# Kernel tuning notes

Measured on AMD Instinct MI355X. Metric: run time of the kernel, lower is better.

Reference implementation:

```python
import jax, jax.numpy as jnp
import numpy as np

N_NODES = 50000
N_EDGES = 800000
D_IN = 128
HID = 128
N_CLASSES = 2
N_GRAPHS = 500
N_LAYERS = 7


def setup_inputs() -> dict:
    key = jax.random.key(0)
    ks = jax.random.split(key, 8)
    x = jax.random.normal(ks[0], (N_NODES, D_IN), dtype=jnp.float32)
    edge_index = jax.random.randint(ks[1], (2, N_EDGES), 0, N_NODES, dtype=jnp.int32)
    batch = jnp.sort(jax.random.randint(ks[2], (N_NODES,), 0, N_GRAPHS, dtype=jnp.int32))
    s = 1.0 / np.sqrt(HID).astype(np.float32)
    # SAGEConv params: Wl (neighbor lin, with bias bl), Wr (root lin, no bias)
    Wl = jax.random.normal(ks[3], (N_LAYERS, HID, HID), dtype=jnp.float32) * s
    Wr = jax.random.normal(ks[4], (N_LAYERS, HID, HID), dtype=jnp.float32) * s
    bl = jnp.zeros((N_LAYERS, HID), dtype=jnp.float32)
    W_out = jax.random.normal(ks[5], (HID, N_CLASSES), dtype=jnp.float32) * s
    b_out = jnp.zeros((N_CLASSES,), dtype=jnp.float32)
    return {"x": x, "edge_index": edge_index, "batch": batch,
            "Wl": Wl, "Wr": Wr, "bl": bl, "W_out": W_out, "b_out": b_out}


def reference(x, edge_index, batch, Wl, Wr, bl, W_out, b_out):
    n = x.shape[0]
    src, dst = edge_index[0], edge_index[1]  # messages flow src -> dst
    deg = jax.ops.segment_sum(jnp.ones_like(dst, dtype=x.dtype), dst, num_segments=n)
    inv_deg = (1.0 / jnp.clip(deg, 1.0))[:, None]  # [N,1]; zero-degree -> aggregate stays 0

    def sage_layer(h, i):
        # mean aggregation of neighbor features, then linear + root linear
        agg = jax.ops.segment_sum(h[src], dst, num_segments=n) * inv_deg  # [N,H]
        return agg @ Wl[i] + bl[i] + h @ Wr[i]

    h = x
    for i in range(N_LAYERS - 1):
        h = jax.nn.relu(sage_layer(h, i))
    h = sage_layer(h, N_LAYERS - 1)  # last conv: no relu

    pooled = jax.ops.segment_sum(h, batch, num_segments=N_GRAPHS)  # global_add_pool
    # F.dropout with training=False is identity (eval mode)
    return pooled @ W_out + b_out  # [G, num_classes]
```

## Files before the change

### kernel.cpp

```cpp
#include <hip/hip_runtime.h>
#include <stdint.h>

#define NN 50000
#define NE 800000
#define HID 128
#define NG 500
#define NL 7

typedef short bf16x8 __attribute__((ext_vector_type(8)));
typedef float f32x4 __attribute__((ext_vector_type(4)));

__device__ __forceinline__ unsigned short f2bf(float f) {
  unsigned int u = __builtin_bit_cast(unsigned int, f);
  u += 0x7FFFu + ((u >> 16) & 1u);
  return (unsigned short)(u >> 16);
}
__device__ __forceinline__ float bf2f(unsigned short h) {
  unsigned int u = ((unsigned int)h) << 16;
  return __builtin_bit_cast(float, u);
}
__device__ __forceinline__ float bflo(unsigned int u) {
  return __builtin_bit_cast(float, u << 16);
}
__device__ __forceinline__ float bfhi(unsigned int u) {
  return __builtin_bit_cast(float, u & 0xffff0000u);
}

__global__ void k_pre(const float* __restrict__ x, unsigned short* __restrict__ hA,
                      unsigned short* __restrict__ hB,
                      const int* __restrict__ dstE, int* __restrict__ deg,
                      const float* __restrict__ Wl, const float* __restrict__ Wr,
                      unsigned short* __restrict__ wswh,
                      unsigned short* __restrict__ wswl) {
  int i = blockIdx.x * 256 + threadIdx.x;
  if (i < NN * HID / 4) {
    float4 v = ((const float4*)x)[i];
    ushort4 r;
    r.x = f2bf(v.x); r.y = f2bf(v.y); r.z = f2bf(v.z); r.w = f2bf(v.w);
    ((ushort4*)hA)[i] = r;
  }
  if (i < NE) atomicAdd(&deg[dstE[i]], 1);
  if (i < NL * 2 * 4 * 4096) {
    int j = i & 7, ii = (i >> 3) & 15, q = (i >> 7) & 3, t = (i >> 9) & 7;
    int cc = (i >> 12) & 3, m = (i >> 14) & 1, l = i >> 15;
    int k = cc * 32 + q * 8 + j, n = t * 16 + ii;
    const float* W = m ? Wr : Wl;
    float w = W[l * HID * HID + k * HID + n];
    unsigned short hi = f2bf(w);
    unsigned short lo = f2bf(w - bf2f(hi));
    wswh[i] = hi;
    wswl[i] = lo;
  }
  if (i < 2048) {
    int b = i >> 10, r = (i >> 4) & 63, u = i & 15;
    unsigned short* pad = (b ? hB : hA) + (size_t)(NN + r) * HID;
    *(uint4*)&pad[u * 8] = make_uint4(0u, 0u, 0u, 0u);
  }
}

__global__ void k_scan1(const int* __restrict__ deg, int* __restrict__ offs,
                        int* __restrict__ bsum) {
  int i = blockIdx.x * 256 + threadIdx.x;
  int v = (i < NN) ? deg[i] : 0;
  int lane = threadIdx.x & 63, wv = threadIdx.x >> 6;
  int x = v;
  #pragma unroll
  for (int d = 1; d < 64; d <<= 1) {
    int y = __shfl_up(x, d, 64);
    if (lane >= d) x += y;
  }
  __shared__ int wsum[4];
  if (lane == 63) wsum[wv] = x;
  __syncthreads();
  if (threadIdx.x == 0) {
    int s = 0;
    for (int k = 0; k < 4; k++) { int t = wsum[k]; wsum[k] = s; s += t; }
    bsum[blockIdx.x] = s;
  }
  __syncthreads();
  if (i < NN) offs[i] = x - v + wsum[wv];
}

__global__ void k_scan2(int* __restrict__ bsum, int nb) {
  int i = threadIdx.x;
  int v = (i < nb) ? bsum[i] : 0;
  int lane = threadIdx.x & 63, wv = threadIdx.x >> 6;
  int x = v;
  #pragma unroll
  for (int d = 1; d < 64; d <<= 1) {
    int y = __shfl_up(x, d, 64);
    if (lane >= d) x += y;
  }
  __shared__ int wsum[4];
  if (lane == 63) wsum[wv] = x;
  __syncthreads();
  if (threadIdx.x == 0) {
    int s = 0;
    for (int k = 0; k < 4; k++) { int t = wsum[k]; wsum[k] = s; s += t; }
  }
  __syncthreads();
  if (i < nb) bsum[i] = x - v + wsum[wv];
}

__global__ void k_scan3(const int* __restrict__ deg, int* __restrict__ offs,
                        const int* __restrict__ bsum, float* __restrict__ invd) {
  int i = blockIdx.x * 256 + threadIdx.x;
  if (i < NN) {
    offs[i] += bsum[blockIdx.x];
    int d = deg[i];
    invd[i] = 1.0f / (float)(d > 0 ? d : 1);
    if (i == 0) offs[NN] = NE;
  }
}

__global__ void k_fill(const int* __restrict__ src, const int* __restrict__ dst,
                       const int* __restrict__ offs, int* __restrict__ cur,
                       int* __restrict__ csr) {
  int e = blockIdx.x * 256 + threadIdx.x;
  if (e < NE) {
    int d = dst[e];
    int p = atomicAdd(&cur[d], 1);
    csr[offs[d] + p] = src[e];
  }
}

#define ACC8(V) { a0 += bflo(V.x); a1 += bfhi(V.x); a2 += bflo(V.y); \
                  a3 += bfhi(V.y); a4 += bflo(V.z); a5 += bfhi(V.z); \
                  a6 += bflo(V.w); a7 += bfhi(V.w); }

__global__ __launch_bounds__(256, 6) void k_agg(const unsigned short* __restrict__ curh,
                                                const int* __restrict__ offs,
                                                const int* __restrict__ csr,
                                                const float* __restrict__ invd,
                                                unsigned short* __restrict__ agg) {
  const int tid = threadIdx.x;
  const int qw = tid >> 4, sl = tid & 15;
  const int node = blockIdx.x * 16 + qw;
  const unsigned short* rowbase = curh + sl * 8;
  float a0 = 0.f, a1 = 0.f, a2 = 0.f, a3 = 0.f;
  float a4 = 0.f, a5 = 0.f, a6 = 0.f, a7 = 0.f;
  const int s = offs[node], e = offs[node + 1];
  for (int base = s; base < e; base += 16) {
    int idx = (base + sl < e) ? csr[base + sl] : NN;
    uint4 v0 = *(const uint4*)(rowbase + (size_t)__shfl(idx, 0, 16) * HID);
    uint4 v1 = *(const uint4*)(rowbase + (size_t)__shfl(idx, 1, 16) * HID);
    uint4 v2 = *(const uint4*)(rowbase + (size_t)__shfl(idx, 2, 16) * HID);
    uint4 v3 = *(const uint4*)(rowbase + (size_t)__shfl(idx, 3, 16) * HID);
    uint4 v4 = *(const uint4*)(rowbase + (size_t)__shfl(idx, 4, 16) * HID);
    uint4 v5 = *(const uint4*)(rowbase + (size_t)__shfl(idx, 5, 16) * HID);
    uint4 v6 = *(const uint4*)(rowbase + (size_t)__shfl(idx, 6, 16) * HID);
    uint4 v7 = *(const uint4*)(rowbase + (size_t)__shfl(idx, 7, 16) * HID);
    ACC8(v0) ACC8(v1) ACC8(v2) ACC8(v3) ACC8(v4) ACC8(v5) ACC8(v6) ACC8(v7)
    if (base + 8 < e) {
      v0 = *(const uint4*)(rowbase + (size_t)__shfl(idx,  8, 16) * HID);
      v1 = *(const uint4*)(rowbase + (size_t)__shfl(idx,  9, 16) * HID);
      v2 = *(const uint4*)(rowbase + (size_t)__shfl(idx, 10, 16) * HID);
      v3 = *(const uint4*)(rowbase + (size_t)__shfl(idx, 11, 16) * HID);
      v4 = *(const uint4*)(rowbase + (size_t)__shfl(idx, 12, 16) * HID);
      v5 = *(const uint4*)(rowbase + (size_t)__shfl(idx, 13, 16) * HID);
      v6 = *(const uint4*)(rowbase + (size_t)__shfl(idx, 14, 16) * HID);
      v7 = *(const uint4*)(rowbase + (size_t)__shfl(idx, 15, 16) * HID);
      ACC8(v0) ACC8(v1) ACC8(v2) ACC8(v3) ACC8(v4) ACC8(v5) ACC8(v6) ACC8(v7)
    }
  }
  float sc = invd[node];
  a0 *= sc; a1 *= sc; a2 *= sc; a3 *= sc;
  a4 *= sc; a5 *= sc; a6 *= sc; a7 *= sc;
  unsigned int w0 = (unsigned int)f2bf(a0) | ((unsigned int)f2bf(a1) << 16);
  unsigned int w1 = (unsigned int)f2bf(a2) | ((unsigned int)f2bf(a3) << 16);
  unsigned int w2 = (unsigned int)f2bf(a4) | ((unsigned int)f2bf(a5) << 16);
  unsigned int w3 = (unsigned int)f2bf(a6) | ((unsigned int)f2bf(a7) << 16);
  *(uint4*)(agg + (size_t)node * HID + sl * 8) = make_uint4(w0, w1, w2, w3);
}

__global__ __launch_bounds__(256) void k_gemm(const unsigned short* __restrict__ agg,
                                              const unsigned short* __restrict__ curh,
                                              const unsigned short* __restrict__ wswh,
                                              const unsigned short* __restrict__ wswl,
                                              const float* __restrict__ bias,
                                              unsigned short* __restrict__ out,
                                              int relu) {
  __shared__ __align__(16) unsigned short sW2[8192];
  const int tid = threadIdx.x;
  const int lane = tid & 63, wv = tid >> 6;
  const int row0 = blockIdx.x * 64;
  const int mr = (wv << 4) + (lane & 15);
  const int q = lane >> 4;
  const unsigned short* aRow = agg + (size_t)(row0 + mr) * HID + q * 8;
  const unsigned short* hRow = curh + (size_t)(row0 + mr) * HID + q * 8;

  f32x4 acc[8];
  #pragma unroll
  for (int t = 0; t < 8; t++) acc[t] = (f32x4){0.f, 0.f, 0.f, 0.f};

  for (int c = 0; c < 8; ++c) {
    const uint4* wh = (const uint4*)(wswh + c * 4096);
    const uint4* wl = (const uint4*)(wswl + c * 4096);
    ((uint4*)sW2)[tid] = wh[tid];
    ((uint4*)sW2)[tid + 256] = wh[tid + 256];
    ((uint4*)sW2)[tid + 512] = wl[tid];
    ((uint4*)sW2)[tid + 768] = wl[tid + 256];
    __syncthreads();
    bf16x8 a = *(const bf16x8*)(((c < 4) ? aRow : hRow) + (c & 3) * 32);
    #pragma unroll
    for (int t = 0; t < 8; t++) {
      bf16x8 bh = *(const bf16x8*)&sW2[(t * 4 + q) * 128 + (lane & 15) * 8];
      bf16x8 bl2 = *(const bf16x8*)&sW2[4096 + (t * 4 + q) * 128 + (lane & 15) * 8];
      acc[t] = __builtin_amdgcn_mfma_f32_16x16x32_bf16(a, bh, acc[t], 0, 0, 0);
      acc[t] = __builtin_amdgcn_mfma_f32_16x16x32_bf16(a, bl2, acc[t], 0, 0, 0);
    }
    __syncthreads();
  }

  const int ci = lane & 15;
  const int rb = (wv << 4) + (lane >> 4) * 4;
  #pragma unroll
  for (int t = 0; t < 8; t++) {
    int n = t * 16 + ci;
    float bn = bias[n];
    #pragma unroll
    for (int r2 = 0; r2 < 4; r2++) {
      int row = row0 + rb + r2;
      if (row < NN) {
        float v = acc[t][r2] + bn;
        if (relu) v = fmaxf(v, 0.f);
        out[(size_t)row * HID + n] = f2bf(v);
      }
    }
  }
}

__global__ void k_pool(const unsigned short* __restrict__ h,
                       const int* __restrict__ batch, float* __restrict__ pooled) {
  int g = blockIdx.x;
  __shared__ int rng[2];
  __shared__ float tmp[HID];
  if (threadIdx.x < 2) {
    int target = g + threadIdx.x;
    int lo = 0, hi = NN;
    while (lo < hi) {
      int mid = (lo + hi) >> 1;
      if (batch[mid] < target) lo = mid + 1; else hi = mid;
    }
    rng[threadIdx.x] = lo;
  }
  __syncthreads();
  int s = rng[0], e = rng[1];
  int f = threadIdx.x & 127, ro = threadIdx.x >> 7;
  float a = 0.f;
  for (int r = s + ro; r < e; r += 2) a += bf2f(h[(size_t)r * HID + f]);
  if (ro == 1) tmp[f] = a;
  __syncthreads();
  if (ro == 0) pooled[g * HID + f] = a + tmp[f];
}

__global__ void k_out(const float* __restrict__ pooled,
                      const float* __restrict__ Wout,
                      const float* __restrict__ bout,
                      float* __restrict__ out) {
  int g = blockIdx.x;
  int l = threadIdx.x;
  float a = pooled[g * HID + l], b = pooled[g * HID + 64 + l];
  float p0 = a * Wout[l * 2] + b * Wout[(l + 64) * 2];
  float p1 = a * Wout[l * 2 + 1] + b * Wout[(l + 64) * 2 + 1];
  #pragma unroll
  for (int d = 32; d; d >>= 1) {
    p0 += __shfl_down(p0, d, 64);
    p1 += __shfl_down(p1, d, 64);
  }
  if (l == 0) {
    out[g * 2] = p0 + bout[0];
    out[g * 2 + 1] = p1 + bout[1];
  }
}

extern "C" void kernel_launch(void* const* d_in, const int* in_sizes, int n_in,
                              void* d_out, int out_size, void* d_ws, size_t ws_size,
                              hipStream_t stream) {
  const float* x = (const float*)d_in[0];
  const int* ei = (const int*)d_in[1];
  const int* batch = (const int*)d_in[2];
  const float* Wl = (const float*)d_in[3];
  const float* Wr = (const float*)d_in[4];
  const float* bl = (const float*)d_in[5];
  const float* Wout = (const float*)d_in[6];
  const float* bout = (const float*)d_in[7];
  float* out = (float*)d_out;
  const int* srcE = ei;
  const int* dstE = ei + NE;

  char* w = (char*)d_ws;
  unsigned short* hA = (unsigned short*)w;  w += (size_t)(NN + 64) * HID * 2;
  unsigned short* hB = (unsigned short*)w;  w += (size_t)(NN + 64) * HID * 2;
  unsigned short* agg = (unsigned short*)w; w += (size_t)(NN + 64) * HID * 2;
  float* invd = (float*)w;   w += (size_t)NN * 4;
  float* pooled = (float*)w; w += (size_t)NG * HID * 4;
  int* deg = (int*)w;  w += (size_t)NN * 4;
  int* cur = (int*)w;  w += (size_t)NN * 4;
  int* offs = (int*)w; w += (size_t)50004 * 4;
  int* csr = (int*)w;  w += (size_t)NE * 4;
  int* bsum = (int*)w; w += 256 * 4;
  unsigned short* wswh = (unsigned short*)w; w += (size_t)NL * 2 * 4 * 4096 * 2;
  unsigned short* wswl = (unsigned short*)w;

  hipMemsetAsync(deg, 0, (size_t)NN * 2 * 4, stream);
  k_pre<<<(NN * HID / 4 + 255) / 256, 256, 0, stream>>>(x, hA, hB, dstE, deg,
                                                        Wl, Wr, wswh, wswl);
  int nb = (NN + 255) / 256;
  k_scan1<<<nb, 256, 0, stream>>>(deg, offs, bsum);
  k_scan2<<<1, 256, 0, stream>>>(bsum, nb);
  k_scan3<<<nb, 256, 0, stream>>>(deg, offs, bsum, invd);
  k_fill<<<(NE + 255) / 256, 256, 0, stream>>>(srcE, dstE, offs, cur, csr);

  unsigned short* curh = hA;
  unsigned short* nxth = hB;
  for (int l = 0; l < NL; l++) {
    k_agg<<<NN / 16, 256, 0, stream>>>(curh, offs, csr, invd, agg);
    k_gemm<<<(NN + 63) / 64, 256, 0, stream>>>(agg, curh,
                                               wswh + (size_t)l * 2 * 4 * 4096,
                                               wswl + (size_t)l * 2 * 4 * 4096,
                                               bl + l * HID, nxth,
                                               (l < NL - 1) ? 1 : 0);
    unsigned short* t = curh; curh = nxth; nxth = t;
  }
  k_pool<<<NG, 256, 0, stream>>>(curh, batch, pooled);
  k_out<<<NG, 64, 0, stream>>>(pooled, Wout, bout, out);
}
```

Before: 545.2 us.

## Partition CSR fill by destination range and issue all 16 gathers per chunk

The CSR fill kernel now splits its 1024 blocks into 128 edge chunks times 8 destination ranges. Each block scans its chunk and only scatters edges whose destination lies in its range, which keeps atomics and csr writes in a narrower address window, at the cost of reading dst eight times. The aggregation kernel now issues all 16 neighbor row loads unconditionally, relying on the padded sentinel row NN, to raise memory-level parallelism. Its occupancy hint drops from 6 to 4 to make room for the extra registers.

```diff
diff --git a/kernel.cpp b/kernel.cpp
--- a/kernel.cpp
+++ b/kernel.cpp
@@ -113,14 +113,20 @@
   }
 }
 
+#define FILL_CHUNK (NE / 128)
 __global__ void k_fill(const int* __restrict__ src, const int* __restrict__ dst,
                        const int* __restrict__ offs, int* __restrict__ cur,
                        int* __restrict__ csr) {
-  int e = blockIdx.x * 256 + threadIdx.x;
-  if (e < NE) {
+  const int r = blockIdx.x & 7;
+  const int chunk = blockIdx.x >> 3;
+  const int lo = r * (NN / 8), hi = lo + (NN / 8);
+  const int e0 = chunk * FILL_CHUNK;
+  for (int e = e0 + threadIdx.x; e < e0 + FILL_CHUNK; e += 256) {
     int d = dst[e];
-    int p = atomicAdd(&cur[d], 1);
-    csr[offs[d] + p] = src[e];
+    if (d >= lo && d < hi) {
+      int p = atomicAdd(&cur[d], 1);
+      csr[offs[d] + p] = src[e];
+    }
   }
 }
 
@@ -128,7 +134,7 @@
                   a3 += bfhi(V.y); a4 += bflo(V.z); a5 += bfhi(V.z); \
                   a6 += bflo(V.w); a7 += bfhi(V.w); }
 
-__global__ __launch_bounds__(256, 6) void k_agg(const unsigned short* __restrict__ curh,
+__global__ __launch_bounds__(256, 4) void k_agg(const unsigned short* __restrict__ curh,
                                                 const int* __restrict__ offs,
                                                 const int* __restrict__ csr,
                                                 const float* __restrict__ invd,
@@ -142,26 +148,26 @@
   const int s = offs[node], e = offs[node + 1];
   for (int base = s; base < e; base += 16) {
     int idx = (base + sl < e) ? csr[base + sl] : NN;
-    uint4 v0 = *(const uint4*)(rowbase + (size_t)__shfl(idx, 0, 16) * HID);
-    uint4 v1 = *(const uint4*)(rowbase + (size_t)__shfl(idx, 1, 16) * HID);
-    uint4 v2 = *(const uint4*)(rowbase + (size_t)__shfl(idx, 2, 16) * HID);
-    uint4 v3 = *(const uint4*)(rowbase + (size_t)__shfl(idx, 3, 16) * HID);
-    uint4 v4 = *(const uint4*)(rowbase + (size_t)__shfl(idx, 4, 16) * HID);
-    uint4 v5 = *(const uint4*)(rowbase + (size_t)__shfl(idx, 5, 16) * HID);
-    uint4 v6 = *(const uint4*)(rowbase + (size_t)__shfl(idx, 6, 16) * HID);
-    uint4 v7 = *(const uint4*)(rowbase + (size_t)__shfl(idx, 7, 16) * HID);
-    ACC8(v0) ACC8(v1) ACC8(v2) ACC8(v3) ACC8(v4) ACC8(v5) ACC8(v6) ACC8(v7)
-    if (base + 8 < e) {
-      v0 = *(const uint4*)(rowbase + (size_t)__shfl(idx,  8, 16) * HID);
-      v1 = *(const uint4*)(rowbase + (size_t)__shfl(idx,  9, 16) * HID);
-      v2 = *(const uint4*)(rowbase + (size_t)__shfl(idx, 10, 16) * HID);
-      v3 = *(const uint4*)(rowbase + (size_t)__shfl(idx, 11, 16) * HID);
-      v4 = *(const uint4*)(rowbase + (size_t)__shfl(idx, 12, 16) * HID);
-      v5 = *(const uint4*)(rowbase + (size_t)__shfl(idx, 13, 16) * HID);
-      v6 = *(const uint4*)(rowbase + (size_t)__shfl(idx, 14, 16) * HID);
-      v7 = *(const uint4*)(rowbase + (size_t)__shfl(idx, 15, 16) * HID);
-      ACC8(v0) ACC8(v1) ACC8(v2) ACC8(v3) ACC8(v4) ACC8(v5) ACC8(v6) ACC8(v7)
-    }
+    uint4 v0  = *(const uint4*)(rowbase + (size_t)__shfl(idx,  0, 16) * HID);
+    uint4 v1  = *(const uint4*)(rowbase + (size_t)__shfl(idx,  1, 16) * HID);
+    uint4 v2  = *(const uint4*)(rowbase + (size_t)__shfl(idx,  2, 16) * HID);
+    uint4 v3  = *(const uint4*)(rowbase + (size_t)__shfl(idx,  3, 16) * HID);
+    uint4 v4  = *(const uint4*)(rowbase + (size_t)__shfl(idx,  4, 16) * HID);
+    uint4 v5  = *(const uint4*)(rowbase + (size_t)__shfl(idx,  5, 16) * HID);
+    uint4 v6  = *(const uint4*)(rowbase + (size_t)__shfl(idx,  6, 16) * HID);
+    uint4 v7  = *(const uint4*)(rowbase + (size_t)__shfl(idx,  7, 16) * HID);
+    uint4 v8  = *(const uint4*)(rowbase + (size_t)__shfl(idx,  8, 16) * HID);
+    uint4 v9  = *(const uint4*)(rowbase + (size_t)__shfl(idx,  9, 16) * HID);
+    uint4 v10 = *(const uint4*)(rowbase + (size_t)__shfl(idx, 10, 16) * HID);
+    uint4 v11 = *(const uint4*)(rowbase + (size_t)__shfl(idx, 11, 16) * HID);
+    uint4 v12 = *(const uint4*)(rowbase + (size_t)__shfl(idx, 12, 16) * HID);
+    uint4 v13 = *(const uint4*)(rowbase + (size_t)__shfl(idx, 13, 16) * HID);
+    uint4 v14 = *(const uint4*)(rowbase + (size_t)__shfl(idx, 14, 16) * HID);
+    uint4 v15 = *(const uint4*)(rowbase + (size_t)__shfl(idx, 15, 16) * HID);
+    ACC8(v0)  ACC8(v1)  ACC8(v2)  ACC8(v3)
+    ACC8(v4)  ACC8(v5)  ACC8(v6)  ACC8(v7)
+    ACC8(v8)  ACC8(v9)  ACC8(v10) ACC8(v11)
+    ACC8(v12) ACC8(v13) ACC8(v14) ACC8(v15)
   }
   float sc = invd[node];
   a0 *= sc; a1 *= sc; a2 *= sc; a3 *= sc;
@@ -310,7 +316,7 @@
   k_scan1<<<nb, 256, 0, stream>>>(deg, offs, bsum);
   k_scan2<<<1, 256, 0, stream>>>(bsum, nb);
   k_scan3<<<nb, 256, 0, stream>>>(deg, offs, bsum, invd);
-  k_fill<<<(NE + 255) / 256, 256, 0, stream>>>(srcE, dstE, offs, cur, csr);
+  k_fill<<<1024, 256, 0, stream>>>(srcE, dstE, offs, cur, csr);
 
   unsigned short* curh = hA;
   unsigned short* nxth = hB;
```

Result: slower. 586.8 us (+7.6%).

## Fuse neighbor aggregation into GEMM kernel via LDS; partition CSR fill by dst range

Applied to the files above, without the earlier changes.

Merges the per-layer aggregation and GEMM kernels into one. Each 64-row block gathers its neighbor means into a swizzled LDS tile and feeds it straight to the MFMA loop, so the bf16 agg buffer is never written to or read back from global memory. The CSR fill now launches 1024 blocks that each scan a chunk of edges and handle only destinations in one eighth of the node range, which localizes the atomics and scattered writes. In exchange, the fused kernel uses 32KB of LDS per block and has fewer blocks than the old aggregation kernel. The fill step also reads the edge list eight times.

```diff
diff --git a/kernel.cpp b/kernel.cpp
--- a/kernel.cpp
+++ b/kernel.cpp
@@ -113,14 +113,20 @@
   }
 }
 
+#define FILL_CHUNK (NE / 128)
 __global__ void k_fill(const int* __restrict__ src, const int* __restrict__ dst,
                        const int* __restrict__ offs, int* __restrict__ cur,
                        int* __restrict__ csr) {
-  int e = blockIdx.x * 256 + threadIdx.x;
-  if (e < NE) {
+  const int r = blockIdx.x & 7;
+  const int chunk = blockIdx.x >> 3;
+  const int lo = r * (NN / 8), hi = lo + (NN / 8);
+  const int e0 = chunk * FILL_CHUNK;
+  for (int e = e0 + threadIdx.x; e < e0 + FILL_CHUNK; e += 256) {
     int d = dst[e];
-    int p = atomicAdd(&cur[d], 1);
-    csr[offs[d] + p] = src[e];
+    if (d >= lo && d < hi) {
+      int p = atomicAdd(&cur[d], 1);
+      csr[offs[d] + p] = src[e];
+    }
   }
 }
 
@@ -128,65 +134,69 @@
                   a3 += bfhi(V.y); a4 += bflo(V.z); a5 += bfhi(V.z); \
                   a6 += bflo(V.w); a7 += bfhi(V.w); }
 
-__global__ __launch_bounds__(256, 6) void k_agg(const unsigned short* __restrict__ curh,
-                                                const int* __restrict__ offs,
-                                                const int* __restrict__ csr,
-                                                const float* __restrict__ invd,
-                                                unsigned short* __restrict__ agg) {
-  const int tid = threadIdx.x;
-  const int qw = tid >> 4, sl = tid & 15;
-  const int node = blockIdx.x * 16 + qw;
-  const unsigned short* rowbase = curh + sl * 8;
-  float a0 = 0.f, a1 = 0.f, a2 = 0.f, a3 = 0.f;
-  float a4 = 0.f, a5 = 0.f, a6 = 0.f, a7 = 0.f;
-  const int s = offs[node], e = offs[node + 1];
-  for (int base = s; base < e; base += 16) {
-    int idx = (base + sl < e) ? csr[base + sl] : NN;
-    uint4 v0 = *(const uint4*)(rowbase + (size_t)__shfl(idx, 0, 16) * HID);
-    uint4 v1 = *(const uint4*)(rowbase + (size_t)__shfl(idx, 1, 16) * HID);
-    uint4 v2 = *(const uint4*)(rowbase + (size_t)__shfl(idx, 2, 16) * HID);
-    uint4 v3 = *(const uint4*)(rowbase + (size_t)__shfl(idx, 3, 16) * HID);
-    uint4 v4 = *(const uint4*)(rowbase + (size_t)__shfl(idx, 4, 16) * HID);
-    uint4 v5 = *(const uint4*)(rowbase + (size_t)__shfl(idx, 5, 16) * HID);
-    uint4 v6 = *(const uint4*)(rowbase + (size_t)__shfl(idx, 6, 16) * HID);
-    uint4 v7 = *(const uint4*)(rowbase + (size_t)__shfl(idx, 7, 16) * HID);
-    ACC8(v0) ACC8(v1) ACC8(v2) ACC8(v3) ACC8(v4) ACC8(v5) ACC8(v6) ACC8(v7)
-    if (base + 8 < e) {
-      v0 = *(const uint4*)(rowbase + (size_t)__shfl(idx,  8, 16) * HID);
-      v1 = *(const uint4*)(rowbase + (size_t)__shfl(idx,  9, 16) * HID);
-      v2 = *(const uint4*)(rowbase + (size_t)__shfl(idx, 10, 16) * HID);
-      v3 = *(const uint4*)(rowbase + (size_t)__shfl(idx, 11, 16) * HID);
-      v4 = *(const uint4*)(rowbase + (size_t)__shfl(idx, 12, 16) * HID);
-      v5 = *(const uint4*)(rowbase + (size_t)__shfl(idx, 13, 16) * HID);
-      v6 = *(const uint4*)(rowbase + (size_t)__shfl(idx, 14, 16) * HID);
-      v7 = *(const uint4*)(rowbase + (size_t)__shfl(idx, 15, 16) * HID);
-      ACC8(v0) ACC8(v1) ACC8(v2) ACC8(v3) ACC8(v4) ACC8(v5) ACC8(v6) ACC8(v7)
-    }
-  }
-  float sc = invd[node];
-  a0 *= sc; a1 *= sc; a2 *= sc; a3 *= sc;
-  a4 *= sc; a5 *= sc; a6 *= sc; a7 *= sc;
-  unsigned int w0 = (unsigned int)f2bf(a0) | ((unsigned int)f2bf(a1) << 16);
-  unsigned int w1 = (unsigned int)f2bf(a2) | ((unsigned int)f2bf(a3) << 16);
-  unsigned int w2 = (unsigned int)f2bf(a4) | ((unsigned int)f2bf(a5) << 16);
-  unsigned int w3 = (unsigned int)f2bf(a6) | ((unsigned int)f2bf(a7) << 16);
-  *(uint4*)(agg + (size_t)node * HID + sl * 8) = make_uint4(w0, w1, w2, w3);
-}
-
-__global__ __launch_bounds__(256) void k_gemm(const unsigned short* __restrict__ agg,
-                                              const unsigned short* __restrict__ curh,
-                                              const unsigned short* __restrict__ wswh,
-                                              const unsigned short* __restrict__ wswl,
-                                              const float* __restrict__ bias,
-                                              unsigned short* __restrict__ out,
-                                              int relu) {
+__global__ __launch_bounds__(256) void k_layer(const unsigned short* __restrict__ curh,
+                                               const int* __restrict__ offs,
+                                               const int* __restrict__ csr,
+                                               const float* __restrict__ invd,
+                                               const unsigned short* __restrict__ wswh,
+                                               const unsigned short* __restrict__ wswl,
+                                               const float* __restrict__ bias,
+                                               unsigned short* __restrict__ out,
+                                               int relu) {
+  __shared__ __align__(16) unsigned short sA[8192];
   __shared__ __align__(16) unsigned short sW2[8192];
   const int tid = threadIdx.x;
+  const int row0 = blockIdx.x * 64;
+
+  {
+    const int qw = tid >> 4, sl = tid & 15;
+    const unsigned short* rowbase = curh + sl * 8;
+    for (int it = 0; it < 4; ++it) {
+      const int lrow = it * 16 + qw;
+      const int node = row0 + lrow;
+      float a0 = 0.f, a1 = 0.f, a2 = 0.f, a3 = 0.f;
+      float a4 = 0.f, a5 = 0.f, a6 = 0.f, a7 = 0.f;
+      if (node < NN) {
+        const int s = offs[node], e = offs[node + 1];
+        for (int base = s; base < e; base += 16) {
+          int idx = (base + sl < e) ? csr[base + sl] : NN;
+          uint4 v0 = *(const uint4*)(rowbase + (size_t)__shfl(idx, 0, 16) * HID);
+          uint4 v1 = *(const uint4*)(rowbase + (size_t)__shfl(idx, 1, 16) * HID);
+          uint4 v2 = *(const uint4*)(rowbase + (size_t)__shfl(idx, 2, 16) * HID);
+          uint4 v3 = *(const uint4*)(rowbase + (size_t)__shfl(idx, 3, 16) * HID);
+          uint4 v4 = *(const uint4*)(rowbase + (size_t)__shfl(idx, 4, 16) * HID);
+          uint4 v5 = *(const uint4*)(rowbase + (size_t)__shfl(idx, 5, 16) * HID);
+          uint4 v6 = *(const uint4*)(rowbase + (size_t)__shfl(idx, 6, 16) * HID);
+          uint4 v7 = *(const uint4*)(rowbase + (size_t)__shfl(idx, 7, 16) * HID);
+          ACC8(v0) ACC8(v1) ACC8(v2) ACC8(v3) ACC8(v4) ACC8(v5) ACC8(v6) ACC8(v7)
+          if (base + 8 < e) {
+            v0 = *(const uint4*)(rowbase + (size_t)__shfl(idx,  8, 16) * HID);
+            v1 = *(const uint4*)(rowbase + (size_t)__shfl(idx,  9, 16) * HID);
+            v2 = *(const uint4*)(rowbase + (size_t)__shfl(idx, 10, 16) * HID);
+            v3 = *(const uint4*)(rowbase + (size_t)__shfl(idx, 11, 16) * HID);
+            v4 = *(const uint4*)(rowbase + (size_t)__shfl(idx, 12, 16) * HID);
+            v5 = *(const uint4*)(rowbase + (size_t)__shfl(idx, 13, 16) * HID);
+            v6 = *(const uint4*)(rowbase + (size_t)__shfl(idx, 14, 16) * HID);
+            v7 = *(const uint4*)(rowbase + (size_t)__shfl(idx, 15, 16) * HID);
+            ACC8(v0) ACC8(v1) ACC8(v2) ACC8(v3) ACC8(v4) ACC8(v5) ACC8(v6) ACC8(v7)
+          }
+        }
+        float sc = invd[node];
+        a0 *= sc; a1 *= sc; a2 *= sc; a3 *= sc;
+        a4 *= sc; a5 *= sc; a6 *= sc; a7 *= sc;
+      }
+      unsigned int w0 = (unsigned int)f2bf(a0) | ((unsigned int)f2bf(a1) << 16);
+      unsigned int w1 = (unsigned int)f2bf(a2) | ((unsigned int)f2bf(a3) << 16);
+      unsigned int w2 = (unsigned int)f2bf(a4) | ((unsigned int)f2bf(a5) << 16);
+      unsigned int w3 = (unsigned int)f2bf(a6) | ((unsigned int)f2bf(a7) << 16);
+      *(uint4*)&sA[lrow * 128 + ((sl ^ (qw & 7)) << 3)] =
+          make_uint4(w0, w1, w2, w3);
+    }
+  }
+
   const int lane = tid & 63, wv = tid >> 6;
-  const int row0 = blockIdx.x * 64;
   const int mr = (wv << 4) + (lane & 15);
   const int q = lane >> 4;
-  const unsigned short* aRow = agg + (size_t)(row0 + mr) * HID + q * 8;
   const unsigned short* hRow = curh + (size_t)(row0 + mr) * HID + q * 8;
 
   f32x4 acc[8];
@@ -201,7 +211,12 @@
     ((uint4*)sW2)[tid + 512] = wl[tid];
     ((uint4*)sW2)[tid + 768] = wl[tid + 256];
     __syncthreads();
-    bf16x8 a = *(const bf16x8*)(((c < 4) ? aRow : hRow) + (c & 3) * 32);
+    bf16x8 a;
+    if (c < 4) {
+      a = *(const bf16x8*)&sA[mr * 128 + (((c * 4 + q) ^ (mr & 7)) << 3)];
+    } else {
+      a = *(const bf16x8*)(hRow + (c & 3) * 32);
+    }
     #pragma unroll
     for (int t = 0; t < 8; t++) {
       bf16x8 bh = *(const bf16x8*)&sW2[(t * 4 + q) * 128 + (lane & 15) * 8];
@@ -292,7 +307,6 @@
   char* w = (char*)d_ws;
   unsigned short* hA = (unsigned short*)w;  w += (size_t)(NN + 64) * HID * 2;
   unsigned short* hB = (unsigned short*)w;  w += (size_t)(NN + 64) * HID * 2;
-  unsigned short* agg = (unsigned short*)w; w += (size_t)(NN + 64) * HID * 2;
   float* invd = (float*)w;   w += (size_t)NN * 4;
   float* pooled = (float*)w; w += (size_t)NG * HID * 4;
   int* deg = (int*)w;  w += (size_t)NN * 4;
@@ -310,17 +324,16 @@
   k_scan1<<<nb, 256, 0, stream>>>(deg, offs, bsum);
   k_scan2<<<1, 256, 0, stream>>>(bsum, nb);
   k_scan3<<<nb, 256, 0, stream>>>(deg, offs, bsum, invd);
-  k_fill<<<(NE + 255) / 256, 256, 0, stream>>>(srcE, dstE, offs, cur, csr);
+  k_fill<<<1024, 256, 0, stream>>>(srcE, dstE, offs, cur, csr);
 
   unsigned short* curh = hA;
   unsigned short* nxth = hB;
   for (int l = 0; l < NL; l++) {
-    k_agg<<<NN / 16, 256, 0, stream>>>(curh, offs, csr, invd, agg);
-    k_gemm<<<(NN + 63) / 64, 256, 0, stream>>>(agg, curh,
-                                               wswh + (size_t)l * 2 * 4 * 4096,
-                                               wswl + (size_t)l * 2 * 4 * 4096,
-                                               bl + l * HID, nxth,
-                                               (l < NL - 1) ? 1 : 0);
+    k_layer<<<(NN + 63) / 64, 256, 0, stream>>>(curh, offs, csr, invd,
+                                                wswh + (size_t)l * 2 * 4 * 4096,
+                                                wswl + (size_t)l * 2 * 4 * 4096,
+                                                bl + l * HID, nxth,
+                                                (l < NL - 1) ? 1 : 0);
     unsigned short* t = curh; curh = nxth; nxth = t;
   }
   k_pool<<<NG, 256, 0, stream>>>(curh, batch, pooled);
```

Measured after the change: 574.6 us. 1.05x slower.
